# Performance work log

Measured on AMD Instinct MI355X. Metric: run time of the kernel, lower is better.

Reference implementation:

```python
import jax, jax.numpy as jnp
import numpy as np

B, T, E, H = 256, 200, 512, 8
NEG = -(2.0 ** 32) + 1.0  # padding value used by the TF implementation


def _pos_table(T, E):
    # sin/cos positional encoding exactly as in PositionEncoding.build
    pos = np.arange(T)[:, None].astype(np.float64)
    i = np.arange(E)[None, :]
    angle = pos / np.power(10000.0, 2.0 * (i // 2) / E)
    pe = np.where(i % 2 == 0, np.sin(angle), np.cos(angle))
    return jnp.asarray(pe, dtype=jnp.float32)


def setup_inputs() -> dict:
    key = jax.random.key(0)
    ks = jax.random.split(key, 9)
    tn = lambda k, shape, std: (jax.random.truncated_normal(k, -2.0, 2.0, shape, jnp.float32) * std)
    glorot = lambda k, shape: jax.random.uniform(k, shape, jnp.float32,
                                                 -np.sqrt(6.0 / (shape[0] + shape[1])),
                                                 np.sqrt(6.0 / (shape[0] + shape[1])))
    return {
        "queries": jax.random.normal(ks[0], (B, T, E), jnp.float32),
        "keys": jax.random.normal(ks[1], (B, T, E), jnp.float32),
        "query_len": jax.random.randint(ks[2], (B, 1), 1, T + 1),
        "key_len": jax.random.randint(ks[3], (B, 1), 1, T + 1),
        "pos_q": _pos_table(T, E),
        "pos_k": _pos_table(T, E),
        "W_Q": tn(ks[4], (E, E), 0.05),
        "W_K": tn(ks[5], (E, E), 0.05),
        "W_V": tn(ks[6], (E, E), 0.05),
        "fw1": glorot(ks[7], (E, 4 * E)),
        "fw2": glorot(ks[8], (4 * E, E)),
    }


def reference(queries, keys, query_len, key_len, pos_q, pos_k, W_Q, W_K, W_V, fw1, fw2):
    Bq, Tq, Eq = queries.shape
    Dh = Eq // H
    dt = queries.dtype
    neg = jnp.asarray(NEG, dt)

    # positional encoding: scaled table added to inputs
    scale = jnp.asarray(Eq, dt) ** 0.5
    q_in = queries + pos_q * scale          # (B,T,E)
    k_in = keys + pos_k * scale

    # sequence masks from lengths (B,1) -> (B,T)
    ar = jnp.arange(Tq)[None, :]
    q_mask = (ar < query_len).astype(dt)
    k_mask = (ar < key_len).astype(dt)

    # projections, split into heads
    Q = (q_in @ W_Q).reshape(Bq, Tq, H, Dh)
    K_ = (k_in @ W_K).reshape(Bq, Tq, H, Dh)
    V = (k_in @ W_V).reshape(Bq, Tq, H, Dh)

    # scaled dot-product attention  (B,H,Tq,Tk)
    scores = jnp.einsum('bqhd,bkhd->bhqk', Q, K_) / jnp.asarray(Dh, dt) ** 0.5
    scores = jnp.where(k_mask[:, None, None, :] > 0, scores, neg)
    # blinding: mask the diagonal (query attends to itself)
    eye = jnp.eye(Tq, dtype=bool)
    scores = jnp.where(eye[None, None], neg, scores)
    scores = scores - jnp.max(scores, axis=-1, keepdims=True)
    attn = jax.nn.softmax(scores, axis=-1)
    attn = attn * q_mask[:, None, :, None]

    out = jnp.einsum('bhqk,bkhd->bqhd', attn, V).reshape(Bq, Tq, Eq)

    # residual (use_res=True), no layer norm (use_layer_norm=False)
    out = out + q_in

    # pointwise feed-forward + residual
    ff = jax.nn.relu(out @ fw1) @ fw2
    out = out + ff

    # output_type == 'mean'
    return jnp.mean(out, axis=1, keepdims=True)  # (B,1,E)
```

## Files before the change

### kernel.cpp

```cpp
#include <hip/hip_runtime.h>

#define B_   256
#define T_   200
#define E_   512
#define H_   8
#define Dh_  64
#define F_   2048
#define M_   (B_ * T_)
#define SCALE 22.62741699796952f
#define NEGV  -4294967296.0f

typedef __attribute__((ext_vector_type(8))) short bf16x8;
typedef __attribute__((ext_vector_type(4))) float f32x4;

__device__ __forceinline__ float bf2f(unsigned short u) {
    union { unsigned u32; float f; } v; v.u32 = ((unsigned)u) << 16; return v.f;
}
__device__ __forceinline__ unsigned short f2bf(float f) {
    union { float f32; unsigned u; } v; v.f32 = f;
    unsigned r = v.u + 0x7FFFu + ((v.u >> 16) & 1u);
    return (unsigned short)(r >> 16);
}
__device__ __forceinline__ unsigned pack_hilo(float f) {
    unsigned short hi = f2bf(f);
    unsigned short lo = f2bf(f - bf2f(hi));
    return (unsigned)hi | ((unsigned)lo << 16);
}
__device__ __forceinline__ void load_lds16(const void* g, void* l) {
    __builtin_amdgcn_global_load_lds(
        (const __attribute__((address_space(1))) unsigned int*)g,
        (__attribute__((address_space(3))) unsigned int*)l, 16, 0, 0);
}

__global__ __launch_bounds__(256) void k_prep(
    float* __restrict__ q, float* __restrict__ k,
    const float* __restrict__ pos_q, const float* __restrict__ pos_k)
{
    const int z = blockIdx.y;
    float* X = z ? k : q;
    const float* Ps = z ? pos_k : pos_q;
    size_t idx = ((size_t)blockIdx.x * 256 + threadIdx.x) * 4;
    int row = (int)(idx >> 9);
    int col = (int)(idx & 511);
    int t = row % T_;
    float4 v = *(const float4*)&X[idx];
    float4 p = *(const float4*)&Ps[(size_t)t * E_ + col];
    uint4 o;
    o.x = pack_hilo(v.x + p.x * SCALE);
    o.y = pack_hilo(v.y + p.y * SCALE);
    o.z = pack_hilo(v.z + p.z * SCALE);
    o.w = pack_hilo(v.w + p.w * SCALE);
    *(uint4*)&X[idx] = o;
}

__global__ __launch_bounds__(256) void k_trw(
    const float* __restrict__ in, unsigned short* __restrict__ oh,
    unsigned short* __restrict__ ol)
{
    const int k0 = blockIdx.x * 64, n0 = blockIdx.y * 64;
    const int tid = threadIdx.x;
    __shared__ unsigned short th[64][65], tl[64][65];
#pragma unroll
    for (int i = 0; i < 16; i++) {
        int e = i * 256 + tid;
        int r = e >> 6, c = e & 63;
        float f = in[(size_t)(k0 + r) * 512 + n0 + c];
        unsigned short h = f2bf(f);
        th[r][c] = h;
        tl[r][c] = f2bf(f - bf2f(h));
    }
    __syncthreads();
#pragma unroll
    for (int i = 0; i < 16; i++) {
        int e = i * 256 + tid;
        int r = e >> 6, c = e & 63;
        oh[(size_t)(n0 + r) * 512 + k0 + c] = th[c][r];
        ol[(size_t)(n0 + r) * 512 + k0 + c] = tl[c][r];
    }
}

template<int K, int NPROD, bool SPLIT, bool FOUT, int SKIPM>
__global__ __launch_bounds__(256) void k_projx(
    const unsigned int* __restrict__ Apk,
    const unsigned short* __restrict__ Bh,
    const unsigned short* __restrict__ Bl,
    unsigned short* __restrict__ Chi,
    unsigned short* __restrict__ Clo,
    const int* __restrict__ slen)
{
    const int N = 512;
    __shared__ alignas(16) unsigned int   Asp[128 * 32];
    __shared__ alignas(16) unsigned short BsH[128 * 32];
    __shared__ alignas(16) unsigned short BsL[(NPROD >= 3) ? 128 * 32 : 8];

    const int tid = threadIdx.x;
    const int w = tid >> 6, lane = tid & 63;
    const int m0 = blockIdx.y * 128, n0 = blockIdx.x * 128;
    const int mr = lane & 15, q4 = lane >> 4;

    if (SKIPM) {
        const int bA = m0 / 200;
        const int bB = (m0 + 127) / 200;
        if (bA == bB) {
            const int len = slen[bA];
            const int t0 = m0 - bA * 200;
            if (t0 >= len && (SKIPM == 1 || len > 1)) {
#pragma unroll
                for (int i = 0; i < 8; i++) {
                    int e = i * 256 + tid;
                    int r = e >> 4, cc = e & 15;
                    *(uint4*)&Chi[(size_t)(m0 + r) * N + n0 + cc * 8] =
                        (uint4){0u, 0u, 0u, 0u};
                    if (SPLIT)
                        *(uint4*)&Clo[(size_t)(m0 + r) * N + n0 + cc * 8] =
                            (uint4){0u, 0u, 0u, 0u};
                }
                return;
            }
        }
    }

    f32x4 acc[4][4];
#pragma unroll
    for (int i = 0; i < 4; i++)
#pragma unroll
        for (int j = 0; j < 4; j++) acc[i][j] = (f32x4){0.f, 0.f, 0.f, 0.f};

    const unsigned int* gA[4];
    unsigned int* lA[4];
#pragma unroll
    for (int it = 0; it < 4; it++) {
        int c = it * 256 + tid;
        int row = c >> 3, cc = c & 7;
        gA[it] = Apk + (size_t)(m0 + row) * K + ((cc ^ (row & 7)) * 4);
        lA[it] = Asp + (size_t)(it * 256 + w * 64) * 4;
    }
    const int c0  = w * 64 + lane;
    const int c1  = 256 + c0;
    const int bm0 = c0 >> 2, bq0 = (c0 & 3) ^ ((bm0 >> 1) & 3);
    const int bm1 = c1 >> 2, bq1 = (c1 & 3) ^ ((bm1 >> 1) & 3);
    const unsigned short* gB0h = Bh + (size_t)(n0 + bm0) * K + bq0 * 8;
    const unsigned short* gB1h = Bh + (size_t)(n0 + bm1) * K + bq1 * 8;
    const unsigned short* gB0l = (NPROD >= 3) ? Bl + (size_t)(n0 + bm0) * K + bq0 * 8 : nullptr;
    const unsigned short* gB1l = (NPROD >= 3) ? Bl + (size_t)(n0 + bm1) * K + bq1 * 8 : nullptr;
    unsigned short* lB0h = BsH + (size_t)(w * 64) * 8;
    unsigned short* lB1h = BsH + (size_t)(256 + w * 64) * 8;
    unsigned short* lB0l = BsL + (size_t)(w * 64) * 8;
    unsigned short* lB1l = BsL + (size_t)(256 + w * 64) * 8;

    int cbf[4];
#pragma unroll
    for (int t4 = 0; t4 < 4; t4++) {
        int nb = (w >> 1) * 64 + t4 * 16 + mr;
        cbf[t4] = nb * 4 + (q4 ^ ((nb >> 1) & 3));
    }
    const int ra_base = (w & 1) * 64;

    for (int k0 = 0; k0 < K; k0 += 32) {
#pragma unroll
        for (int it = 0; it < 4; it++) load_lds16(gA[it] + k0, lA[it]);
        load_lds16(gB0h + k0, lB0h);
        load_lds16(gB1h + k0, lB1h);
        if (NPROD >= 3) {
            load_lds16(gB0l + k0, lB0l);
            load_lds16(gB1l + k0, lB1l);
        }
        __syncthreads();

        bf16x8 afh[4], afl[4], bgh[4], bgl[4];
#pragma unroll
        for (int t4 = 0; t4 < 4; t4++) {
            const int ra = ra_base + t4 * 16 + mr;
            const int r7 = ra & 7;
            uint4 u0 = *(const uint4*)&Asp[(size_t)(ra * 8 + ((q4 * 2) ^ r7)) * 4];
            uint4 u1 = *(const uint4*)&Asp[(size_t)(ra * 8 + ((q4 * 2 + 1) ^ r7)) * 4];
            union { unsigned u[4]; bf16x8 v; } Hh, Ll;
            Hh.u[0] = (u0.x & 0xffffu) | (u0.y << 16);
            Hh.u[1] = (u0.z & 0xffffu) | (u0.w << 16);
            Hh.u[2] = (u1.x & 0xffffu) | (u1.y << 16);
            Hh.u[3] = (u1.z & 0xffffu) | (u1.w << 16);
            afh[t4] = Hh.v;
            Ll.u[0] = (u0.x >> 16) | (u0.y & 0xffff0000u);
            Ll.u[1] = (u0.z >> 16) | (u0.w & 0xffff0000u);
            Ll.u[2] = (u1.x >> 16) | (u1.y & 0xffff0000u);
            Ll.u[3] = (u1.z >> 16) | (u1.w & 0xffff0000u);
            afl[t4] = Ll.v;
            bgh[t4] = *(const bf16x8*)&BsH[cbf[t4] * 8];
            if (NPROD >= 3) bgl[t4] = *(const bf16x8*)&BsL[cbf[t4] * 8];
        }
#pragma unroll
        for (int i = 0; i < 4; i++)
#pragma unroll
            for (int j = 0; j < 4; j++) {
                acc[i][j] = __builtin_amdgcn_mfma_f32_16x16x32_bf16(
                    afh[i], bgh[j], acc[i][j], 0, 0, 0);
                if (NPROD >= 3)
                    acc[i][j] = __builtin_amdgcn_mfma_f32_16x16x32_bf16(
                        afh[i], bgl[j], acc[i][j], 0, 0, 0);
                acc[i][j] = __builtin_amdgcn_mfma_f32_16x16x32_bf16(
                    afl[i], bgh[j], acc[i][j], 0, 0, 0);
            }
        __syncthreads();
    }

#pragma unroll
    for (int i = 0; i < 4; i++) {
        int row = m0 + (w & 1) * 64 + i * 16 + (lane >> 4) * 4;
#pragma unroll
        for (int j = 0; j < 4; j++) {
            int col = n0 + (w >> 1) * 64 + j * 16 + mr;
#pragma unroll
            for (int r = 0; r < 4; r++) {
                float v = acc[i][j][r];
                if (FOUT) {
                    ((float*)Chi)[(size_t)(row + r) * N + col] = v;
                } else {
                    unsigned short hi = f2bf(v);
                    Chi[(size_t)(row + r) * N + col] = hi;
                    if (SPLIT)
                        Clo[(size_t)(row + r) * N + col] = f2bf(v - bf2f(hi));
                }
            }
        }
    }
}

__global__ __launch_bounds__(512, 4) void k_attn_flash(
    const unsigned short* __restrict__ Qhi, const unsigned short* __restrict__ Qlo,
    const unsigned short* __restrict__ Khi, const unsigned short* __restrict__ Klo,
    const int* __restrict__ qlen, const int* __restrict__ klen,
    const unsigned int* __restrict__ Apk,
    unsigned short* VX)
{
    const int bh = blockIdx.x;
    const int b = bh >> 3, h = bh & 7;
    const int tid = threadIdx.x;
    const int w = tid >> 6, l = tid & 63;
    const int mr = l & 15, q4 = l >> 4;

    __shared__ alignas(16) unsigned short Kh_s[2][64 * 72];
    __shared__ alignas(16) unsigned short Kl_s[2][64 * 72];
    __shared__ alignas(16) unsigned short Vt_s[2][64 * 72];
    __shared__ alignas(16) unsigned short P_s[8][16 * 72];

    const int kl = klen[b], ql = qlen[b];
    const int cmax = (kl > 1) ? ((kl + 63) >> 6) : 4;

    auto stage = [&](int cs, int sb) {
#pragma unroll
        for (int ii = 0; ii < 2; ii++) {
            const int idx = ii * 512 + tid;
            const int jn = idx >> 4, dq = idx & 15;
            const int n = cs * 64 + jn;
            if (n < T_) {
                const size_t g = (size_t)(b * T_ + n) * E_ + h * 64 + dq * 4;
                *(uint2*)&Kh_s[sb][jn * 72 + dq * 4] = *(const uint2*)&Khi[g];
                *(uint2*)&Kl_s[sb][jn * 72 + dq * 4] = *(const uint2*)&Klo[g];
                ushort4 v = *(const ushort4*)&VX[g];
                Vt_s[sb][(dq * 4 + 0) * 72 + jn] = v.x;
                Vt_s[sb][(dq * 4 + 1) * 72 + jn] = v.y;
                Vt_s[sb][(dq * 4 + 2) * 72 + jn] = v.z;
                Vt_s[sb][(dq * 4 + 3) * 72 + jn] = v.w;
            } else {
                Vt_s[sb][(dq * 4 + 0) * 72 + jn] = 0;
                Vt_s[sb][(dq * 4 + 1) * 72 + jn] = 0;
                Vt_s[sb][(dq * 4 + 2) * 72 + jn] = 0;
                Vt_s[sb][(dq * 4 + 3) * 72 + jn] = 0;
            }
        }
    };

    bf16x8 qh0[2], qh1[2];
#pragma unroll
    for (int j = 0; j < 2; j++) {
        const int qt = w + 8 * j;
        if (qt < 13 && qt * 16 < ql) {
            const size_t qoff = (size_t)(b * T_ + qt * 16 + mr) * E_ + h * 64 + q4 * 8;
            qh0[j] = *(const bf16x8*)&Qhi[qoff];
            qh1[j] = *(const bf16x8*)&Qhi[qoff + 32];
        }
    }

    f32x4 O[2][4];
    float m_r[2][4], l_r[2][4];
#pragma unroll
    for (int j = 0; j < 2; j++) {
#pragma unroll
        for (int nt = 0; nt < 4; nt++) O[j][nt] = (f32x4){0.f, 0.f, 0.f, 0.f};
#pragma unroll
        for (int r = 0; r < 4; r++) { m_r[j][r] = -INFINITY; l_r[j][r] = 0.f; }
    }

    stage(0, 0);
    __syncthreads();

    for (int c = 0; c < cmax; c++) {
        const int pb = c & 1;
        if (c + 1 < cmax) stage(c + 1, pb ^ 1);

#pragma unroll
        for (int j = 0; j < 2; j++) {
            const int qt = w + 8 * j;
            if (qt < 13 && qt * 16 < ql) {
                const int q0 = qt * 16;
                const size_t qoff = (size_t)(b * T_ + q0 + mr) * E_ + h * 64 + q4 * 8;
                bf16x8 qe0 = *(const bf16x8*)&Qlo[qoff];
                bf16x8 qe1 = *(const bf16x8*)&Qlo[qoff + 32];

                f32x4 a[4];
#pragma unroll
                for (int kt = 0; kt < 4; kt++) a[kt] = (f32x4){0.f, 0.f, 0.f, 0.f};
                __builtin_amdgcn_s_setprio(1);
#pragma unroll
                for (int kt = 0; kt < 4; kt++) {
                    if (c * 64 + kt * 16 < 208) {
                        const int rbase = (kt * 16 + mr) * 72 + q4 * 8;
                        bf16x8 kh0 = *(const bf16x8*)&Kh_s[pb][rbase];
                        bf16x8 kh1 = *(const bf16x8*)&Kh_s[pb][rbase + 32];
                        bf16x8 ke0 = *(const bf16x8*)&Kl_s[pb][rbase];
                        bf16x8 ke1 = *(const bf16x8*)&Kl_s[pb][rbase + 32];
                        a[kt] = __builtin_amdgcn_mfma_f32_16x16x32_bf16(qh0[j], kh0, a[kt], 0, 0, 0);
                        a[kt] = __builtin_amdgcn_mfma_f32_16x16x32_bf16(qh1[j], kh1, a[kt], 0, 0, 0);
                        a[kt] = __builtin_amdgcn_mfma_f32_16x16x32_bf16(qh0[j], ke0, a[kt], 0, 0, 0);
                        a[kt] = __builtin_amdgcn_mfma_f32_16x16x32_bf16(qh1[j], ke1, a[kt], 0, 0, 0);
                        a[kt] = __builtin_amdgcn_mfma_f32_16x16x32_bf16(qe0, kh0, a[kt], 0, 0, 0);
                        a[kt] = __builtin_amdgcn_mfma_f32_16x16x32_bf16(qe1, kh1, a[kt], 0, 0, 0);
                    }
                }
                __builtin_amdgcn_s_setprio(0);

                float mc[4] = {-INFINITY, -INFINITY, -INFINITY, -INFINITY};
#pragma unroll
                for (int kt = 0; kt < 4; kt++) {
                    int col = c * 64 + kt * 16 + mr;
#pragma unroll
                    for (int r = 0; r < 4; r++) {
                        int row = q0 + q4 * 4 + r;
                        float v = a[kt][r] * 0.125f;
                        if (col >= kl)  v = NEGV;
                        if (col == row) v = NEGV;
                        if (col >= T_)  v = -INFINITY;
                        a[kt][r] = v;
                        mc[r] = fmaxf(mc[r], v);
                    }
                }
#pragma unroll
                for (int r = 0; r < 4; r++)
#pragma unroll
                    for (int off = 1; off < 16; off <<= 1)
                        mc[r] = fmaxf(mc[r], __shfl_xor(mc[r], off));
                float mn[4], alpha[4], ps[4];
#pragma unroll
                for (int r = 0; r < 4; r++) {
                    mn[r] = fmaxf(m_r[j][r], mc[r]);
                    alpha[r] = __expf(m_r[j][r] - mn[r]);
                    ps[r] = 0.f;
                }
#pragma unroll
                for (int kt = 0; kt < 4; kt++)
#pragma unroll
                    for (int r = 0; r < 4; r++) {
                        float p = __expf(a[kt][r] - mn[r]);
                        a[kt][r] = p;
                        ps[r] += p;
                    }
#pragma unroll
                for (int r = 0; r < 4; r++)
#pragma unroll
                    for (int off = 1; off < 16; off <<= 1)
                        ps[r] += __shfl_xor(ps[r], off);
#pragma unroll
                for (int r = 0; r < 4; r++) {
                    l_r[j][r] = l_r[j][r] * alpha[r] + ps[r];
                    m_r[j][r] = mn[r];
                }
#pragma unroll
                for (int nt = 0; nt < 4; nt++)
#pragma unroll
                    for (int r = 0; r < 4; r++) O[j][nt][r] *= alpha[r];
#pragma unroll
                for (int kt = 0; kt < 4; kt++)
#pragma unroll
                    for (int r = 0; r < 4; r++)
                        P_s[w][(q4 * 4 + r) * 72 + kt * 16 + mr] = f2bf(a[kt][r]);
                __builtin_amdgcn_s_setprio(1);
#pragma unroll
                for (int k2 = 0; k2 < 2; k2++) {
                    bf16x8 pf = *(const bf16x8*)&P_s[w][mr * 72 + k2 * 32 + q4 * 8];
#pragma unroll
                    for (int nt = 0; nt < 4; nt++) {
                        bf16x8 vf = *(const bf16x8*)&Vt_s[pb][(nt * 16 + mr) * 72 + k2 * 32 + q4 * 8];
                        O[j][nt] = __builtin_amdgcn_mfma_f32_16x16x32_bf16(pf, vf, O[j][nt], 0, 0, 0);
                    }
                }
                __builtin_amdgcn_s_setprio(0);
            }
        }
        __syncthreads();
    }

#pragma unroll
    for (int j = 0; j < 2; j++) {
        const int qt = w + 8 * j;
        if (qt < 13) {
#pragma unroll
            for (int r = 0; r < 4; r++) {
                int row = qt * 16 + q4 * 4 + r;
                if (row < T_) {
                    float inv = (row < ql) ? (1.f / l_r[j][r]) : 0.f;
#pragma unroll
                    for (int nt = 0; nt < 4; nt++) {
                        int d = nt * 16 + mr;
                        size_t gi = (size_t)(b * T_ + row) * E_ + h * 64 + d;
                        unsigned u = Apk[gi];
                        float res = bf2f((unsigned short)(u & 0xffff)) +
                                    bf2f((unsigned short)(u >> 16));
                        VX[gi] = f2bf(O[j][nt][r] * inv + res);
                    }
                }
            }
        }
    }
}

__global__ __launch_bounds__(256) void k_tr(
    const float* __restrict__ in, unsigned short* __restrict__ out, int K, int N)
{
    const int k0 = blockIdx.x * 64, n0 = blockIdx.y * 64;
    const int tid = threadIdx.x;
    __shared__ unsigned short t[64][65];
#pragma unroll
    for (int i = 0; i < 16; i++) {
        int e = i * 256 + tid;
        int r = e >> 6, c = e & 63;
        t[r][c] = f2bf(in[(size_t)(k0 + r) * N + n0 + c]);
    }
    __syncthreads();
#pragma unroll
    for (int i = 0; i < 16; i++) {
        int e = i * 256 + tid;
        int r = e >> 6, c = e & 63;
        out[(size_t)(n0 + r) * K + k0 + c] = t[c][r];
    }
}

__global__ __launch_bounds__(256) void k_gemm_relusum(
    const unsigned short* __restrict__ A,
    const unsigned short* __restrict__ Bt,
    float* __restrict__ Hsum)
{
    const int K = E_, N = F_;
    __shared__ alignas(16) unsigned short As[2][128 * 32];
    __shared__ alignas(16) unsigned short Bs[2][128 * 32];
    __shared__ float colsum[2][128];

    const int tid  = threadIdx.x;
    const int w    = tid >> 6, lane = tid & 63;
    const int m0   = blockIdx.y * 128, n0 = blockIdx.x * 128;
    const int mr   = lane & 15, q = lane >> 4;

    f32x4 acc[4][4];
#pragma unroll
    for (int i = 0; i < 4; i++)
#pragma unroll
        for (int j = 0; j < 4; j++) acc[i][j] = (f32x4){0.f, 0.f, 0.f, 0.f};

    const int c0  = w * 64 + lane;
    const int c1  = 256 + w * 64 + lane;
    const int am0 = c0 >> 2, aq0 = (c0 & 3) ^ ((am0 >> 1) & 3);
    const int am1 = c1 >> 2, aq1 = (c1 & 3) ^ ((am1 >> 1) & 3);
    const unsigned short* gA0 = A  + (size_t)(m0 + am0) * K + aq0 * 8;
    const unsigned short* gA1 = A  + (size_t)(m0 + am1) * K + aq1 * 8;
    const unsigned short* gB0 = Bt + (size_t)(n0 + am0) * K + aq0 * 8;
    const unsigned short* gB1 = Bt + (size_t)(n0 + am1) * K + aq1 * 8;
    unsigned short* lA0[2] = { As[0] + (size_t)(w * 64) * 8, As[1] + (size_t)(w * 64) * 8 };
    unsigned short* lA1[2] = { As[0] + (size_t)(256 + w * 64) * 8, As[1] + (size_t)(256 + w * 64) * 8 };
    unsigned short* lB0[2] = { Bs[0] + (size_t)(w * 64) * 8, Bs[1] + (size_t)(w * 64) * 8 };
    unsigned short* lB1[2] = { Bs[0] + (size_t)(256 + w * 64) * 8, Bs[1] + (size_t)(256 + w * 64) * 8 };

    int caf[4], cbf[4];
#pragma unroll
    for (int t4 = 0; t4 < 4; t4++) {
        int ma = (w & 1) * 64 + t4 * 16 + mr;
        caf[t4] = ma * 4 + (q ^ ((ma >> 1) & 3));
        int nb = (w >> 1) * 64 + t4 * 16 + mr;
        cbf[t4] = nb * 4 + (q ^ ((nb >> 1) & 3));
    }

    for (int k0 = 0; k0 < K; k0 += 64) {
#pragma unroll
        for (int hh = 0; hh < 2; hh++) {
            load_lds16(gA0 + k0 + hh * 32, lA0[hh]);
            load_lds16(gA1 + k0 + hh * 32, lA1[hh]);
            load_lds16(gB0 + k0 + hh * 32, lB0[hh]);
            load_lds16(gB1 + k0 + hh * 32, lB1[hh]);
        }
        __syncthreads();

#pragma unroll
        for (int hh = 0; hh < 2; hh++) {
            bf16x8 af[4], bg[4];
#pragma unroll
            for (int t4 = 0; t4 < 4; t4++) {
                af[t4] = *(const bf16x8*)&As[hh][caf[t4] * 8];
                bg[t4] = *(const bf16x8*)&Bs[hh][cbf[t4] * 8];
            }
#pragma unroll
            for (int i = 0; i < 4; i++)
#pragma unroll
                for (int j = 0; j < 4; j++)
                    acc[i][j] = __builtin_amdgcn_mfma_f32_16x16x32_bf16(
                        af[i], bg[j], acc[i][j], 0, 0, 0);
        }
        __syncthreads();
    }

    ((float*)colsum)[tid] = 0.f;
    __syncthreads();
    const int b0 = m0 / 200;
    const int bsplit = (b0 + 1) * 200;
#pragma unroll
    for (int j = 0; j < 4; j++) {
        const int colr = (w >> 1) * 64 + j * 16 + mr;
        float s0 = 0.f, s1 = 0.f;
#pragma unroll
        for (int i = 0; i < 4; i++) {
            const int rowb = m0 + (w & 1) * 64 + i * 16 + q * 4;
#pragma unroll
            for (int r = 0; r < 4; r++) {
                float v = fmaxf(acc[i][j][r], 0.f);
                if (rowb + r >= bsplit) s1 += v; else s0 += v;
            }
        }
        atomicAdd(&colsum[0][colr], s0);
        atomicAdd(&colsum[1][colr], s1);
    }
    __syncthreads();
    if (tid < 128) {
        atomicAdd(&Hsum[(size_t)b0 * N + n0 + tid], colsum[0][tid]);
        if (bsplit < m0 + 128)
            atomicAdd(&Hsum[(size_t)(b0 + 1) * N + n0 + tid], colsum[1][tid]);
    }
}

__global__ __launch_bounds__(256) void k_zero(float* __restrict__ p)
{
    ((float4*)p)[(size_t)blockIdx.x * 256 + threadIdx.x] = (float4){0.f, 0.f, 0.f, 0.f};
}

__global__ __launch_bounds__(256) void k_hm(
    const float* __restrict__ Hsum, unsigned int* __restrict__ Hmpk)
{
    size_t idx = ((size_t)blockIdx.x * 256 + threadIdx.x) * 4;
    float4 v = *(const float4*)&Hsum[idx];
    uint4 o;
    o.x = pack_hilo(v.x * (1.0f / 200.0f));
    o.y = pack_hilo(v.y * (1.0f / 200.0f));
    o.z = pack_hilo(v.z * (1.0f / 200.0f));
    o.w = pack_hilo(v.w * (1.0f / 200.0f));
    *(uint4*)&Hmpk[idx] = o;
}

__global__ __launch_bounds__(256) void k_final(
    const unsigned short* __restrict__ X, const float* __restrict__ ffm,
    float* __restrict__ out)
{
    const int b = blockIdx.x;
    const int w = threadIdx.x >> 6, lane = threadIdx.x & 63;
    float s[8] = {0.f, 0.f, 0.f, 0.f, 0.f, 0.f, 0.f, 0.f};
    for (int t = w; t < T_; t += 4) {
        bf16x8 v = *(const bf16x8*)&X[(size_t)(b * T_ + t) * E_ + lane * 8];
#pragma unroll
        for (int j = 0; j < 8; j++) s[j] += bf2f((unsigned short)v[j]);
    }
    __shared__ float red[4][512];
#pragma unroll
    for (int j = 0; j < 8; j++) red[w][lane * 8 + j] = s[j];
    __syncthreads();
    for (int e = threadIdx.x; e < 512; e += 256)
        out[(size_t)b * E_ + e] =
            (red[0][e] + red[1][e] + red[2][e] + red[3][e]) * (1.0f / 200.0f) +
            ffm[(size_t)b * E_ + e];
}

extern "C" void kernel_launch(void* const* d_in, const int* in_sizes, int n_in,
                              void* d_out, int out_size, void* d_ws, size_t ws_size,
                              hipStream_t stream)
{
    float* qmut = (float*)d_in[0];
    float* kmut = (float*)d_in[1];
    const int*   qlen  = (const int*)d_in[2];
    const int*   klen  = (const int*)d_in[3];
    const float* pos_q = (const float*)d_in[4];
    const float* pos_k = (const float*)d_in[5];
    const float* W_Q   = (const float*)d_in[6];
    const float* W_K   = (const float*)d_in[7];
    const float* W_V   = (const float*)d_in[8];
    const float* fw1   = (const float*)d_in[9];
    const float* fw2   = (const float*)d_in[10];
    float* out = (float*)d_out;

    char* base = (char*)d_ws;
    unsigned short* Qhi = (unsigned short*)base;
    unsigned short* Qlo = (unsigned short*)(base +  52428800);
    unsigned short* Khi = (unsigned short*)(base + 104857600);
    unsigned short* Klo = (unsigned short*)(base + 157286400);
    unsigned short* VX  = (unsigned short*)(base + 209715200);

    unsigned short* wQh = VX;
    unsigned short* wQl = VX + 262144;
    unsigned short* wKh = VX + 524288;
    unsigned short* wKl = VX + 786432;
    unsigned short* wVh = (unsigned short*)W_Q;
    unsigned short* wVl = (unsigned short*)W_Q + 262144;

    unsigned short* fw1t = (unsigned short*)(base + 157286400);
    unsigned short* fw2t = (unsigned short*)(base + 159383552);
    float*        Hsum = (float*)(base + 161480704);
    unsigned int* Hmpk = (unsigned int*)(base + 163577856);
    float*        ffm  = (float*)(base + 165675008);

    const unsigned int* Aq = (const unsigned int*)qmut;
    const unsigned int* Ak = (const unsigned int*)kmut;

    k_prep<<<dim3(M_ * E_ / 1024, 2), 256, 0, stream>>>(qmut, kmut, pos_q, pos_k);
    k_trw<<<dim3(8, 8), 256, 0, stream>>>(W_Q, wQh, wQl);
    k_trw<<<dim3(8, 8), 256, 0, stream>>>(W_K, wKh, wKl);
    k_projx<512, 3, true, false, 1><<<dim3(4, M_ / 128), 256, 0, stream>>>(
        Aq, wQh, wQl, Qhi, Qlo, qlen);
    k_projx<512, 3, true, false, 1><<<dim3(4, M_ / 128), 256, 0, stream>>>(
        Ak, wKh, wKl, Khi, Klo, klen);
    k_trw<<<dim3(8, 8), 256, 0, stream>>>(W_V, wVh, wVl);
    k_projx<512, 2, false, false, 2><<<dim3(4, M_ / 128), 256, 0, stream>>>(
        Ak, wVh, nullptr, VX, nullptr, klen);

    k_attn_flash<<<B_ * H_, 512, 0, stream>>>(
        Qhi, Qlo, Khi, Klo, qlen, klen, Aq, VX);

    k_tr<<<dim3(E_ / 64, F_ / 64), 256, 0, stream>>>(fw1, fw1t, E_, F_);
    k_tr<<<dim3(F_ / 64, E_ / 64), 256, 0, stream>>>(fw2, fw2t, F_, E_);
    k_zero<<<512, 256, 0, stream>>>(Hsum);

    k_gemm_relusum<<<dim3(F_ / 128, M_ / 128), 256, 0, stream>>>(VX, fw1t, Hsum);
    k_hm<<<512, 256, 0, stream>>>(Hsum, Hmpk);
    k_projx<2048, 2, false, true, 0><<<dim3(4, 2), 256, 0, stream>>>(
        Hmpk, fw2t, nullptr, (unsigned short*)ffm, nullptr, nullptr);
    k_final<<<B_, 256, 0, stream>>>(VX, ffm, out);
}
```

Measured before the change: 954.9 us.

## Remap GEMM blocks across XCDs and shrink relu-sum K step to 32

Replaces 2D grids with 1D grids and remaps block IDs so that consecutive tiles are grouped per XCD, which is meant to improve L2 reuse of A/B tiles on the multi-die MI355X. The FFN relu-sum GEMM also drops from a 64-wide K step (two LDS halves) to a 32-wide step with half the LDS. This lowers LDS use and may raise occupancy, at the cost of twice as many barriers per K loop. The final small projection has 8 blocks, so the swizzle degenerates to the identity there.

```diff
diff --git a/kernel.cpp b/kernel.cpp
--- a/kernel.cpp
+++ b/kernel.cpp
@@ -30,6 +30,10 @@
     __builtin_amdgcn_global_load_lds(
         (const __attribute__((address_space(1))) unsigned int*)g,
         (__attribute__((address_space(3))) unsigned int*)l, 16, 0, 0);
+}
+__device__ __forceinline__ int xcd_swz(int bid, int nwg) {
+    int cpx = nwg >> 3;
+    return (bid & 7) * cpx + (bid >> 3);
 }
 
 __global__ __launch_bounds__(256) void k_prep(
@@ -79,7 +83,7 @@
     }
 }
 
-template<int K, int NPROD, bool SPLIT, bool FOUT, int SKIPM>
+template<int K, int NPROD, bool SPLIT, bool FOUT, int SKIPM, int NT>
 __global__ __launch_bounds__(256) void k_projx(
     const unsigned int* __restrict__ Apk,
     const unsigned short* __restrict__ Bh,
@@ -95,7 +99,8 @@
 
     const int tid = threadIdx.x;
     const int w = tid >> 6, lane = tid & 63;
-    const int m0 = blockIdx.y * 128, n0 = blockIdx.x * 128;
+    const int swz = xcd_swz(blockIdx.x, gridDim.x);
+    const int m0 = (swz / NT) * 128, n0 = (swz % NT) * 128;
     const int mr = lane & 15, q4 = lane >> 4;
 
     if (SKIPM) {
@@ -450,13 +455,14 @@
     float* __restrict__ Hsum)
 {
     const int K = E_, N = F_;
-    __shared__ alignas(16) unsigned short As[2][128 * 32];
-    __shared__ alignas(16) unsigned short Bs[2][128 * 32];
+    __shared__ alignas(16) unsigned short As[128 * 32];
+    __shared__ alignas(16) unsigned short Bs[128 * 32];
     __shared__ float colsum[2][128];
 
     const int tid  = threadIdx.x;
     const int w    = tid >> 6, lane = tid & 63;
-    const int m0   = blockIdx.y * 128, n0 = blockIdx.x * 128;
+    const int swz  = xcd_swz(blockIdx.x, gridDim.x);
+    const int m0   = (swz >> 4) * 128, n0 = (swz & 15) * 128;
     const int mr   = lane & 15, q = lane >> 4;
 
     f32x4 acc[4][4];
@@ -473,10 +479,10 @@
     const unsigned short* gA1 = A  + (size_t)(m0 + am1) * K + aq1 * 8;
     const unsigned short* gB0 = Bt + (size_t)(n0 + am0) * K + aq0 * 8;
     const unsigned short* gB1 = Bt + (size_t)(n0 + am1) * K + aq1 * 8;
-    unsigned short* lA0[2] = { As[0] + (size_t)(w * 64) * 8, As[1] + (size_t)(w * 64) * 8 };
-    unsigned short* lA1[2] = { As[0] + (size_t)(256 + w * 64) * 8, As[1] + (size_t)(256 + w * 64) * 8 };
-    unsigned short* lB0[2] = { Bs[0] + (size_t)(w * 64) * 8, Bs[1] + (size_t)(w * 64) * 8 };
-    unsigned short* lB1[2] = { Bs[0] + (size_t)(256 + w * 64) * 8, Bs[1] + (size_t)(256 + w * 64) * 8 };
+    unsigned short* lA0 = As + (size_t)(w * 64) * 8;
+    unsigned short* lA1 = As + (size_t)(256 + w * 64) * 8;
+    unsigned short* lB0 = Bs + (size_t)(w * 64) * 8;
+    unsigned short* lB1 = Bs + (size_t)(256 + w * 64) * 8;
 
     int caf[4], cbf[4];
 #pragma unroll
@@ -487,31 +493,25 @@
         cbf[t4] = nb * 4 + (q ^ ((nb >> 1) & 3));
     }
 
-    for (int k0 = 0; k0 < K; k0 += 64) {
-#pragma unroll
-        for (int hh = 0; hh < 2; hh++) {
-            load_lds16(gA0 + k0 + hh * 32, lA0[hh]);
-            load_lds16(gA1 + k0 + hh * 32, lA1[hh]);
-            load_lds16(gB0 + k0 + hh * 32, lB0[hh]);
-            load_lds16(gB1 + k0 + hh * 32, lB1[hh]);
-        }
+    for (int k0 = 0; k0 < K; k0 += 32) {
+        load_lds16(gA0 + k0, lA0);
+        load_lds16(gA1 + k0, lA1);
+        load_lds16(gB0 + k0, lB0);
+        load_lds16(gB1 + k0, lB1);
         __syncthreads();
 
-#pragma unroll
-        for (int hh = 0; hh < 2; hh++) {
-            bf16x8 af[4], bg[4];
-#pragma unroll
-            for (int t4 = 0; t4 < 4; t4++) {
-                af[t4] = *(const bf16x8*)&As[hh][caf[t4] * 8];
-                bg[t4] = *(const bf16x8*)&Bs[hh][cbf[t4] * 8];
-            }
-#pragma unroll
-            for (int i = 0; i < 4; i++)
-#pragma unroll
-                for (int j = 0; j < 4; j++)
-                    acc[i][j] = __builtin_amdgcn_mfma_f32_16x16x32_bf16(
-                        af[i], bg[j], acc[i][j], 0, 0, 0);
-        }
+        bf16x8 af[4], bg[4];
+#pragma unroll
+        for (int t4 = 0; t4 < 4; t4++) {
+            af[t4] = *(const bf16x8*)&As[caf[t4] * 8];
+            bg[t4] = *(const bf16x8*)&Bs[cbf[t4] * 8];
+        }
+#pragma unroll
+        for (int i = 0; i < 4; i++)
+#pragma unroll
+            for (int j = 0; j < 4; j++)
+                acc[i][j] = __builtin_amdgcn_mfma_f32_16x16x32_bf16(
+                    af[i], bg[j], acc[i][j], 0, 0, 0);
         __syncthreads();
     }
 
@@ -626,12 +626,12 @@
     k_prep<<<dim3(M_ * E_ / 1024, 2), 256, 0, stream>>>(qmut, kmut, pos_q, pos_k);
     k_trw<<<dim3(8, 8), 256, 0, stream>>>(W_Q, wQh, wQl);
     k_trw<<<dim3(8, 8), 256, 0, stream>>>(W_K, wKh, wKl);
-    k_projx<512, 3, true, false, 1><<<dim3(4, M_ / 128), 256, 0, stream>>>(
+    k_projx<512, 3, true, false, 1, 4><<<4 * (M_ / 128), 256, 0, stream>>>(
         Aq, wQh, wQl, Qhi, Qlo, qlen);
-    k_projx<512, 3, true, false, 1><<<dim3(4, M_ / 128), 256, 0, stream>>>(
+    k_projx<512, 3, true, false, 1, 4><<<4 * (M_ / 128), 256, 0, stream>>>(
         Ak, wKh, wKl, Khi, Klo, klen);
     k_trw<<<dim3(8, 8), 256, 0, stream>>>(W_V, wVh, wVl);
-    k_projx<512, 2, false, false, 2><<<dim3(4, M_ / 128), 256, 0, stream>>>(
+    k_projx<512, 2, false, false, 2, 4><<<4 * (M_ / 128), 256, 0, stream>>>(
         Ak, wVh, nullptr, VX, nullptr, klen);
 
     k_attn_flash<<<B_ * H_, 512, 0, stream>>>(
@@ -641,9 +641,9 @@
     k_tr<<<dim3(F_ / 64, E_ / 64), 256, 0, stream>>>(fw2, fw2t, F_, E_);
     k_zero<<<512, 256, 0, stream>>>(Hsum);
 
-    k_gemm_relusum<<<dim3(F_ / 128, M_ / 128), 256, 0, stream>>>(VX, fw1t, Hsum);
+    k_gemm_relusum<<<16 * (M_ / 128), 256, 0, stream>>>(VX, fw1t, Hsum);
     k_hm<<<512, 256, 0, stream>>>(Hsum, Hmpk);
-    k_projx<2048, 2, false, true, 0><<<dim3(4, 2), 256, 0, stream>>>(
+    k_projx<2048, 2, false, true, 0, 4><<<8, 256, 0, stream>>>(
         Hmpk, fw2t, nullptr, (unsigned short*)ffm, nullptr, nullptr);
     k_final<<<B_, 256, 0, stream>>>(VX, ffm, out);
 }
```

Result: faster. 924.4 us (-3.2%).
